# Kernel tuning notes

Measured on AMD Instinct MI355X. Metric: run time of the kernel, lower is better.

Reference implementation:

```python
import jax, jax.numpy as jnp
import numpy as np

K = 8
NUM_BLOCKS = 12

def knn_idx(xyz, k):
    # xyz: (B,3,N). kNN in Euclidean space (self included), like gutil.group.
    sq = jnp.sum(xyz * xyz, axis=1)                      # (B,N)
    inner = jnp.einsum('bdn,bdm->bnm', xyz, xyz)         # (B,N,N)
    dist = sq[:, :, None] - 2.0 * inner + sq[:, None, :]
    _, idx = jax.lax.top_k(-dist, k)                     # (B,N,k)
    return idx

def gather_neighbors(points, idx):
    # points: (B,d,N), idx: (B,N,k) -> grouped (B,d,k,N)  [gutil.group_point]
    g = jax.vmap(lambda p, i: p[:, i])(points, idx)      # (B,d,N,k)
    return jnp.transpose(g, (0, 1, 3, 2))

def setup_inputs() -> dict:
    key = jax.random.key(0)
    ks = jax.random.split(key, 6)
    B, N, D = 4, 4096, 128
    return {
        'xyz': jax.random.normal(ks[0], (B, 3, N), dtype=jnp.float32),
        'points': jax.random.normal(ks[1], (B, D, N), dtype=jnp.float32),
        'conv_w1': jax.random.normal(ks[2], (NUM_BLOCKS, D, D), dtype=jnp.float32) * 0.05,
        'conv_w2': jax.random.normal(ks[3], (NUM_BLOCKS, D, D), dtype=jnp.float32) * 0.05,
        'w_center': jax.random.normal(ks[4], (6, D), dtype=jnp.float32) * 0.05,
        'w_neighbor': jax.random.normal(ks[5], (6, D), dtype=jnp.float32) * 0.05,
    }

def reference(xyz, points, conv_w1, conv_w2, w_center, w_neighbor):
    # kNN indices depend only on xyz -> computed once (idx==0 branch in torch).
    idx = knn_idx(xyz, K)
    inv = 1.0 / (K + 1)
    for i in range(NUM_BLOCKS):
        shortcut = points
        p = jax.nn.relu(points)                              # (B,d,N)
        grouped = gather_neighbors(p, idx)                   # (B,d,K,N)
        center = jnp.einsum('oi,bin->bon', conv_w1[i], p)    # 1x1 conv on center
        gnn_sum = jnp.einsum('oi,bikn->bon', conv_w2[i], grouped)  # conv + sum over K
        # mean over concat([center(1), grouped(K)]) along neighbor dim + residual
        points = (center + gnn_sum) * inv + shortcut
        if i == NUM_BLOCKS - 1:
            pxyz = jnp.einsum('oi,bin->bon', w_center, p)            # (B,6,N)
            gxyz_sum = jnp.einsum('oi,bikn->bon', w_neighbor, grouped)
            new_xyz = (pxyz + gxyz_sum) * inv                        # (B,6,N)
            B, _, N = xyz.shape
            new_xyz = new_xyz.reshape(B, 3, 2, N) + xyz[:, :, None, :]
            new_xyz = new_xyz.reshape(B, 3, 2 * N)
            return (new_xyz, points)
```

## Files before the change

kernel.cpp:

```cpp
#include <hip/hip_runtime.h>
#include <math.h>

#define BB 4
#define NN 4096
#define DD 128
#define KK 8
#define NBLK 12

typedef __attribute__((ext_vector_type(8))) short short8;
typedef __attribute__((ext_vector_type(4))) float f32x4;

__device__ inline ushort bf16_rn(float x) {
    uint u = __float_as_uint(x);
    u = (u + 0x7FFFu + ((u >> 16) & 1u)) >> 16;
    return (ushort)u;
}
__device__ inline float bf16_f(ushort h) { return __uint_as_float(((uint)h) << 16); }

__global__ __launch_bounds__(512) void knn_kernel(const float* __restrict__ xyz,
                                                  int* __restrict__ idx) {
    __shared__ float xs[NN], ys[NN], zs[NN];
    const int b = blockIdx.y;
    const float* xb = xyz + (size_t)b * 3 * NN;
    for (int i = threadIdx.x; i < NN; i += 512) {
        xs[i] = xb[i];
        ys[i] = xb[NN + i];
        zs[i] = xb[2 * NN + i];
    }
    __syncthreads();

    const int wave = threadIdx.x >> 6;
    const int lane = threadIdx.x & 63;
    const int n = blockIdx.x * 8 + wave;
    const float qx = xs[n], qy = ys[n], qz = zs[n];
    const float qsq = __fadd_rn(__fadd_rn(__fmul_rn(qx, qx), __fmul_rn(qy, qy)),
                                __fmul_rn(qz, qz));

    float d[KK];
    int id[KK];
#pragma unroll
    for (int j = 0; j < KK; ++j) { d[j] = INFINITY; id[j] = -1; }

    for (int j = 0; j < NN / 256; ++j) {
        const int m0 = j * 256 + lane * 4;
        const float4 vx = *(const float4*)&xs[m0];
        const float4 vy = *(const float4*)&ys[m0];
        const float4 vz = *(const float4*)&zs[m0];
#pragma unroll
        for (int e = 0; e < 4; ++e) {
            const float cx = (&vx.x)[e], cy = (&vy.x)[e], cz = (&vz.x)[e];
            const float cq = __fadd_rn(__fadd_rn(__fmul_rn(cx, cx),
                                                 __fmul_rn(cy, cy)),
                                       __fmul_rn(cz, cz));
            float inner = __fadd_rn(__fadd_rn(__fmul_rn(qx, cx),
                                              __fmul_rn(qy, cy)),
                                    __fmul_rn(qz, cz));
            float dist = __fadd_rn(__fsub_rn(qsq, __fmul_rn(2.0f, inner)), cq);
            if (dist < d[KK - 1]) {
                d[KK - 1] = dist; id[KK - 1] = m0 + e;
#pragma unroll
                for (int t = KK - 1; t > 0; --t) {
                    if (d[t] < d[t - 1]) {
                        float td = d[t]; d[t] = d[t - 1]; d[t - 1] = td;
                        int ti = id[t]; id[t] = id[t - 1]; id[t - 1] = ti;
                    }
                }
            }
        }
    }

    int out[KK];
#pragma unroll
    for (int it = 0; it < KK; ++it) {
        float hd = d[0];
        int hi = id[0];
#pragma unroll
        for (int s = 32; s; s >>= 1) {
            float od = __shfl_xor(hd, s, 64);
            int oi = __shfl_xor(hi, s, 64);
            if (od < hd || (od == hd && oi < hi)) { hd = od; hi = oi; }
        }
        out[it] = hi;
        if (hd == d[0] && hi == id[0]) {
#pragma unroll
            for (int t = 0; t < KK - 1; ++t) { d[t] = d[t + 1]; id[t] = id[t + 1]; }
            d[KK - 1] = INFINITY; id[KK - 1] = -1;
        }
    }

    if (lane == 0) {
        int* op = idx + ((size_t)b * NN + n) * KK;
        *(int4*)op       = make_int4(out[0], out[1], out[2], out[3]);
        *(int4*)(op + 4) = make_int4(out[4], out[5], out[6], out[7]);
    }
}

__global__ __launch_bounds__(256) void prep_w(const float* __restrict__ w1,
                                              const float* __restrict__ w2,
                                              ushort* __restrict__ whi,
                                              ushort* __restrict__ wlo) {
    const int e = blockIdx.x * 256 + threadIdx.x;
    const int l = e >> 15;
    const int rem = e & 32767;
    const int r = rem >> 8;
    const int k = rem & 255;
    float w = (k < 128) ? w1[((size_t)l * 128 + r) * 128 + k]
                        : w2[((size_t)l * 128 + r) * 128 + (k - 128)];
    ushort h = bf16_rn(w);
    whi[e] = h;
    wlo[e] = bf16_rn(w - bf16_f(h));
}

__global__ __launch_bounds__(256) void transpose_pts(const float* __restrict__ pts,
                                                     float* __restrict__ ptsT) {
    __shared__ float t[32][33];
    const int b = blockIdx.z;
    const int c0 = blockIdx.y * 32;
    const int n0 = blockIdx.x * 32;
    const int tx = threadIdx.x & 31;
    const int ty = threadIdx.x >> 5;
#pragma unroll
    for (int q = 0; q < 4; ++q)
        t[ty + 8 * q][tx] = pts[((size_t)b * DD + c0 + ty + 8 * q) * NN + n0 + tx];
    __syncthreads();
#pragma unroll
    for (int q = 0; q < 4; ++q)
        ptsT[((size_t)b * NN + n0 + ty + 8 * q) * DD + c0 + tx] = t[tx][ty + 8 * q];
}

__global__ __launch_bounds__(512, 4) void fused_block(const float* __restrict__ ptsT_in,
                                                      const int* __restrict__ idx,
                                                      const ushort* __restrict__ whi,
                                                      const ushort* __restrict__ wlo,
                                                      float* __restrict__ ptsT_out,
                                                      float* __restrict__ out_std,
                                                      const float* __restrict__ wc,
                                                      const float* __restrict__ wn,
                                                      const float* __restrict__ xyz,
                                                      float* __restrict__ out_xyz,
                                                      const int last) {
    __shared__ __align__(16) char xt[32768];
    __shared__ float sc[32][132];
    char* xt_hi = xt;
    char* xt_lo = xt + 16384;

    const int bid = blockIdx.x;
    const int xcd = bid & 7;
    const int b = xcd >> 1;
    const int colbase = (((xcd & 1) << 6) + (bid >> 3)) * 32;

    const int w = threadIdx.x >> 6;
    const int lane = threadIdx.x & 63;
    const int half = lane >> 5;
    const int l32 = lane & 31;
    const int choff = 4 * l32;
    const int row0 = w * 4;

    const float* baseT = ptsT_in + (size_t)b * NN * DD;

    const int iv = idx[((size_t)b * NN + colbase + row0) * KK + (lane & 31)];

    const int ln15 = lane & 15;
    const int kl = lane >> 4;

#pragma unroll
    for (int i = 0; i < 2; ++i) {
        const int n_loc = row0 + 2 * i + half;
        const int n = colbase + n_loc;

        int nb[KK];
#pragma unroll
        for (int j = 0; j < KK; ++j) nb[j] = __shfl(iv, (2 * i + half) * 8 + j, 64);

        const float4 c4 = *(const float4*)(baseT + (size_t)n * DD + choff);
        float4 u[KK];
#pragma unroll
        for (int j = 0; j < KK; ++j)
            u[j] = *(const float4*)(baseT + (size_t)nb[j] * DD + choff);

        float g0 = 0.f, g1 = 0.f, g2 = 0.f, g3 = 0.f;
#pragma unroll
        for (int j = 0; j < KK; ++j) {
            g0 += fmaxf(u[j].x, 0.f);
            g1 += fmaxf(u[j].y, 0.f);
            g2 += fmaxf(u[j].z, 0.f);
            g3 += fmaxf(u[j].w, 0.f);
        }
        const float p0 = fmaxf(c4.x, 0.f);
        const float p1 = fmaxf(c4.y, 0.f);
        const float p2 = fmaxf(c4.z, 0.f);
        const float p3 = fmaxf(c4.w, 0.f);

        *(float4*)&sc[n_loc][choff] = c4;

        ushort ph0 = bf16_rn(p0), ph1 = bf16_rn(p1), ph2 = bf16_rn(p2), ph3 = bf16_rn(p3);
        ushort pl0 = bf16_rn(p0 - bf16_f(ph0)), pl1 = bf16_rn(p1 - bf16_f(ph1));
        ushort pl2 = bf16_rn(p2 - bf16_f(ph2)), pl3 = bf16_rn(p3 - bf16_f(ph3));
        ushort gh0 = bf16_rn(g0), gh1 = bf16_rn(g1), gh2 = bf16_rn(g2), gh3 = bf16_rn(g3);
        ushort gl0 = bf16_rn(g0 - bf16_f(gh0)), gl1 = bf16_rn(g1 - bf16_f(gh1));
        ushort gl2 = bf16_rn(g2 - bf16_f(gh2)), gl3 = bf16_rn(g3 - bf16_f(gh3));

        const int gP = l32 >> 1;
        const int sub = (l32 & 1) << 3;
        const int byP = n_loc * 512 + ((gP ^ (n_loc & 7)) << 4) + sub;
        const int byG = n_loc * 512 + (((16 + gP) ^ (n_loc & 7)) << 4) + sub;

        *(unsigned long long*)(xt_hi + byP) =
            (unsigned long long)ph0 | ((unsigned long long)ph1 << 16) |
            ((unsigned long long)ph2 << 32) | ((unsigned long long)ph3 << 48);
        *(unsigned long long*)(xt_lo + byP) =
            (unsigned long long)pl0 | ((unsigned long long)pl1 << 16) |
            ((unsigned long long)pl2 << 32) | ((unsigned long long)pl3 << 48);
        *(unsigned long long*)(xt_hi + byG) =
            (unsigned long long)gh0 | ((unsigned long long)gh1 << 16) |
            ((unsigned long long)gh2 << 32) | ((unsigned long long)gh3 << 48);
        *(unsigned long long*)(xt_lo + byG) =
            (unsigned long long)gl0 | ((unsigned long long)gl1 << 16) |
            ((unsigned long long)gl2 << 32) | ((unsigned long long)gl3 << 48);

        if (last) {
            float s0, s1, s2, s3, s4, s5;
            {
                const int c0 = choff, c1 = choff + 1, c2 = choff + 2, c3 = choff + 3;
                s0 = p0 * wc[0 * 128 + c0] + p1 * wc[0 * 128 + c1] + p2 * wc[0 * 128 + c2] + p3 * wc[0 * 128 + c3]
                   + g0 * wn[0 * 128 + c0] + g1 * wn[0 * 128 + c1] + g2 * wn[0 * 128 + c2] + g3 * wn[0 * 128 + c3];
                s1 = p0 * wc[1 * 128 + c0] + p1 * wc[1 * 128 + c1] + p2 * wc[1 * 128 + c2] + p3 * wc[1 * 128 + c3]
                   + g0 * wn[1 * 128 + c0] + g1 * wn[1 * 128 + c1] + g2 * wn[1 * 128 + c2] + g3 * wn[1 * 128 + c3];
                s2 = p0 * wc[2 * 128 + c0] + p1 * wc[2 * 128 + c1] + p2 * wc[2 * 128 + c2] + p3 * wc[2 * 128 + c3]
                   + g0 * wn[2 * 128 + c0] + g1 * wn[2 * 128 + c1] + g2 * wn[2 * 128 + c2] + g3 * wn[2 * 128 + c3];
                s3 = p0 * wc[3 * 128 + c0] + p1 * wc[3 * 128 + c1] + p2 * wc[3 * 128 + c2] + p3 * wc[3 * 128 + c3]
                   + g0 * wn[3 * 128 + c0] + g1 * wn[3 * 128 + c1] + g2 * wn[3 * 128 + c2] + g3 * wn[3 * 128 + c3];
                s4 = p0 * wc[4 * 128 + c0] + p1 * wc[4 * 128 + c1] + p2 * wc[4 * 128 + c2] + p3 * wc[4 * 128 + c3]
                   + g0 * wn[4 * 128 + c0] + g1 * wn[4 * 128 + c1] + g2 * wn[4 * 128 + c2] + g3 * wn[4 * 128 + c3];
                s5 = p0 * wc[5 * 128 + c0] + p1 * wc[5 * 128 + c1] + p2 * wc[5 * 128 + c2] + p3 * wc[5 * 128 + c3]
                   + g0 * wn[5 * 128 + c0] + g1 * wn[5 * 128 + c1] + g2 * wn[5 * 128 + c2] + g3 * wn[5 * 128 + c3];
            }
#pragma unroll
            for (int st = 16; st; st >>= 1) {
                s0 += __shfl_xor(s0, st, 64);
                s1 += __shfl_xor(s1, st, 64);
                s2 += __shfl_xor(s2, st, 64);
                s3 += __shfl_xor(s3, st, 64);
                s4 += __shfl_xor(s4, st, 64);
                s5 += __shfl_xor(s5, st, 64);
            }
            if (l32 < 6) {
                float v = s0;
                v = (l32 == 1) ? s1 : v;
                v = (l32 == 2) ? s2 : v;
                v = (l32 == 3) ? s3 : v;
                v = (l32 == 4) ? s4 : v;
                v = (l32 == 5) ? s5 : v;
                const int dd = l32 >> 1, h = l32 & 1;
                const float xv = xyz[((size_t)b * 3 + dd) * NN + n];
                out_xyz[(((size_t)b * 3 + dd) * 2 + h) * NN + n] =
                    v * (1.0f / 9.0f) + xv;
            }
        }
    }
    __syncthreads();

    const int wrow = w * 16 + ln15;
    f32x4 acc[2] = {};
#pragma unroll
    for (int ks = 0; ks < 8; ++ks) {
        const short8 a_hi = *(const short8*)(whi + (size_t)wrow * 256 + ks * 32 + kl * 8);
        const short8 a_lo = *(const short8*)(wlo + (size_t)wrow * 256 + ks * 32 + kl * 8);
        short8 bfh[2], bfl[2];
#pragma unroll
        for (int nt = 0; nt < 2; ++nt) {
            const int n_loc = nt * 16 + ln15;
            const int by = n_loc * 512 + (((ks * 4 + kl) ^ (n_loc & 7)) << 4);
            bfh[nt] = *(const short8*)(xt_hi + by);
            bfl[nt] = *(const short8*)(xt_lo + by);
        }
#pragma unroll
        for (int nt = 0; nt < 2; ++nt) {
            acc[nt] = __builtin_amdgcn_mfma_f32_16x16x32_bf16(a_hi, bfh[nt], acc[nt], 0, 0, 0);
            acc[nt] = __builtin_amdgcn_mfma_f32_16x16x32_bf16(a_hi, bfl[nt], acc[nt], 0, 0, 0);
            acc[nt] = __builtin_amdgcn_mfma_f32_16x16x32_bf16(a_lo, bfh[nt], acc[nt], 0, 0, 0);
        }
    }

    const float inv = 1.0f / 9.0f;
    const int orow = w * 16 + kl * 4;
#pragma unroll
    for (int nt = 0; nt < 2; ++nt) {
        const int nl = nt * 16 + ln15;
        const int n = colbase + nl;
        const float4 scv = *(const float4*)&sc[nl][orow];
        float v0 = acc[nt][0] * inv + scv.x;
        float v1 = acc[nt][1] * inv + scv.y;
        float v2 = acc[nt][2] * inv + scv.z;
        float v3 = acc[nt][3] * inv + scv.w;
        if (!last) {
            *(float4*)(ptsT_out + ((size_t)b * NN + n) * DD + orow) =
                make_float4(v0, v1, v2, v3);
        } else {
            out_std[((size_t)b * DD + orow + 0) * NN + n] = v0;
            out_std[((size_t)b * DD + orow + 1) * NN + n] = v1;
            out_std[((size_t)b * DD + orow + 2) * NN + n] = v2;
            out_std[((size_t)b * DD + orow + 3) * NN + n] = v3;
        }
    }
}

extern "C" void kernel_launch(void* const* d_in, const int* in_sizes, int n_in,
                              void* d_out, int out_size, void* d_ws, size_t ws_size,
                              hipStream_t stream) {
    const float* xyz    = (const float*)d_in[0];
    const float* points = (const float*)d_in[1];
    const float* w1     = (const float*)d_in[2];
    const float* w2     = (const float*)d_in[3];
    const float* wc     = (const float*)d_in[4];
    const float* wn     = (const float*)d_in[5];
    float* out = (float*)d_out;

    const size_t feat = (size_t)BB * DD * NN;
    char* ws = (char*)d_ws;
    int*    idx  = (int*)ws;
    ushort* whi  = (ushort*)(ws + 524288);
    ushort* wlo  = (ushort*)(ws + 524288 + 786432);
    float*  pT0  = (float*)(ws + 524288 + 2 * 786432);
    float*  pT1  = pT0 + feat;

    knn_kernel<<<dim3(NN / 8, BB), 512, 0, stream>>>(xyz, idx);
    prep_w<<<dim3(12 * 128 * 256 / 256), 256, 0, stream>>>(w1, w2, whi, wlo);
    transpose_pts<<<dim3(NN / 32, DD / 32, BB), 256, 0, stream>>>(points, pT0);

    float* out_pts = out + (size_t)BB * 3 * 2 * NN;
    float* bufs[2] = {pT0, pT1};
    for (int i = 0; i < NBLK; ++i) {
        const int last = (i == NBLK - 1);
        fused_block<<<dim3(512), 512, 0, stream>>>(
            bufs[i & 1], idx, whi + (size_t)i * 32768, wlo + (size_t)i * 32768,
            bufs[(i + 1) & 1], out_pts, wc, wn, xyz, out, last);
    }
}
```

Before: 276.5 us.

## Fuse twelve block launches into one persistent kernel with per-batch grid barriers

Replaces the twelve separate fused_block launches with a single persistent kernel that loops over the blocks internally. Between iterations, the workgroups for each batch synchronise through an atomic counter barrier in global memory, which replaces the kernel-launch boundaries. The goal is to remove launch overhead and the gaps between launches. It depends on all 512 workgroups being resident at the same time (a deadlock risk otherwise), and each barrier adds spin-wait latency plus a memset of the counters.

```diff
diff --git a/kernel.cpp b/kernel.cpp
--- a/kernel.cpp
+++ b/kernel.cpp
@@ -128,17 +128,17 @@
         ptsT[((size_t)b * NN + n0 + ty + 8 * q) * DD + c0 + tx] = t[tx][ty + 8 * q];
 }
 
-__global__ __launch_bounds__(512, 4) void fused_block(const float* __restrict__ ptsT_in,
+__global__ __launch_bounds__(512, 4) void fused_chain(float* __restrict__ pT0,
+                                                      float* __restrict__ pT1,
                                                       const int* __restrict__ idx,
                                                       const ushort* __restrict__ whi,
                                                       const ushort* __restrict__ wlo,
-                                                      float* __restrict__ ptsT_out,
                                                       float* __restrict__ out_std,
                                                       const float* __restrict__ wc,
                                                       const float* __restrict__ wn,
                                                       const float* __restrict__ xyz,
                                                       float* __restrict__ out_xyz,
-                                                      const int last) {
+                                                      unsigned int* ctr) {
     __shared__ __align__(16) char xt[32768];
     __shared__ float sc[32][132];
     char* xt_hi = xt;
@@ -156,151 +156,169 @@
     const int choff = 4 * l32;
     const int row0 = w * 4;
 
-    const float* baseT = ptsT_in + (size_t)b * NN * DD;
-
     const int iv = idx[((size_t)b * NN + colbase + row0) * KK + (lane & 31)];
 
     const int ln15 = lane & 15;
     const int kl = lane >> 4;
 
-#pragma unroll
-    for (int i = 0; i < 2; ++i) {
-        const int n_loc = row0 + 2 * i + half;
-        const int n = colbase + n_loc;
-
-        int nb[KK];
-#pragma unroll
-        for (int j = 0; j < KK; ++j) nb[j] = __shfl(iv, (2 * i + half) * 8 + j, 64);
-
-        const float4 c4 = *(const float4*)(baseT + (size_t)n * DD + choff);
-        float4 u[KK];
-#pragma unroll
-        for (int j = 0; j < KK; ++j)
-            u[j] = *(const float4*)(baseT + (size_t)nb[j] * DD + choff);
-
-        float g0 = 0.f, g1 = 0.f, g2 = 0.f, g3 = 0.f;
-#pragma unroll
-        for (int j = 0; j < KK; ++j) {
-            g0 += fmaxf(u[j].x, 0.f);
-            g1 += fmaxf(u[j].y, 0.f);
-            g2 += fmaxf(u[j].z, 0.f);
-            g3 += fmaxf(u[j].w, 0.f);
-        }
-        const float p0 = fmaxf(c4.x, 0.f);
-        const float p1 = fmaxf(c4.y, 0.f);
-        const float p2 = fmaxf(c4.z, 0.f);
-        const float p3 = fmaxf(c4.w, 0.f);
-
-        *(float4*)&sc[n_loc][choff] = c4;
-
-        ushort ph0 = bf16_rn(p0), ph1 = bf16_rn(p1), ph2 = bf16_rn(p2), ph3 = bf16_rn(p3);
-        ushort pl0 = bf16_rn(p0 - bf16_f(ph0)), pl1 = bf16_rn(p1 - bf16_f(ph1));
-        ushort pl2 = bf16_rn(p2 - bf16_f(ph2)), pl3 = bf16_rn(p3 - bf16_f(ph3));
-        ushort gh0 = bf16_rn(g0), gh1 = bf16_rn(g1), gh2 = bf16_rn(g2), gh3 = bf16_rn(g3);
-        ushort gl0 = bf16_rn(g0 - bf16_f(gh0)), gl1 = bf16_rn(g1 - bf16_f(gh1));
-        ushort gl2 = bf16_rn(g2 - bf16_f(gh2)), gl3 = bf16_rn(g3 - bf16_f(gh3));
-
-        const int gP = l32 >> 1;
-        const int sub = (l32 & 1) << 3;
-        const int byP = n_loc * 512 + ((gP ^ (n_loc & 7)) << 4) + sub;
-        const int byG = n_loc * 512 + (((16 + gP) ^ (n_loc & 7)) << 4) + sub;
-
-        *(unsigned long long*)(xt_hi + byP) =
-            (unsigned long long)ph0 | ((unsigned long long)ph1 << 16) |
-            ((unsigned long long)ph2 << 32) | ((unsigned long long)ph3 << 48);
-        *(unsigned long long*)(xt_lo + byP) =
-            (unsigned long long)pl0 | ((unsigned long long)pl1 << 16) |
-            ((unsigned long long)pl2 << 32) | ((unsigned long long)pl3 << 48);
-        *(unsigned long long*)(xt_hi + byG) =
-            (unsigned long long)gh0 | ((unsigned long long)gh1 << 16) |
-            ((unsigned long long)gh2 << 32) | ((unsigned long long)gh3 << 48);
-        *(unsigned long long*)(xt_lo + byG) =
-            (unsigned long long)gl0 | ((unsigned long long)gl1 << 16) |
-            ((unsigned long long)gl2 << 32) | ((unsigned long long)gl3 << 48);
-
-        if (last) {
-            float s0, s1, s2, s3, s4, s5;
-            {
-                const int c0 = choff, c1 = choff + 1, c2 = choff + 2, c3 = choff + 3;
-                s0 = p0 * wc[0 * 128 + c0] + p1 * wc[0 * 128 + c1] + p2 * wc[0 * 128 + c2] + p3 * wc[0 * 128 + c3]
-                   + g0 * wn[0 * 128 + c0] + g1 * wn[0 * 128 + c1] + g2 * wn[0 * 128 + c2] + g3 * wn[0 * 128 + c3];
-                s1 = p0 * wc[1 * 128 + c0] + p1 * wc[1 * 128 + c1] + p2 * wc[1 * 128 + c2] + p3 * wc[1 * 128 + c3]
-                   + g0 * wn[1 * 128 + c0] + g1 * wn[1 * 128 + c1] + g2 * wn[1 * 128 + c2] + g3 * wn[1 * 128 + c3];
-                s2 = p0 * wc[2 * 128 + c0] + p1 * wc[2 * 128 + c1] + p2 * wc[2 * 128 + c2] + p3 * wc[2 * 128 + c3]
-                   + g0 * wn[2 * 128 + c0] + g1 * wn[2 * 128 + c1] + g2 * wn[2 * 128 + c2] + g3 * wn[2 * 128 + c3];
-                s3 = p0 * wc[3 * 128 + c0] + p1 * wc[3 * 128 + c1] + p2 * wc[3 * 128 + c2] + p3 * wc[3 * 128 + c3]
-                   + g0 * wn[3 * 128 + c0] + g1 * wn[3 * 128 + c1] + g2 * wn[3 * 128 + c2] + g3 * wn[3 * 128 + c3];
-                s4 = p0 * wc[4 * 128 + c0] + p1 * wc[4 * 128 + c1] + p2 * wc[4 * 128 + c2] + p3 * wc[4 * 128 + c3]
-                   + g0 * wn[4 * 128 + c0] + g1 * wn[4 * 128 + c1] + g2 * wn[4 * 128 + c2] + g3 * wn[4 * 128 + c3];
-                s5 = p0 * wc[5 * 128 + c0] + p1 * wc[5 * 128 + c1] + p2 * wc[5 * 128 + c2] + p3 * wc[5 * 128 + c3]
-                   + g0 * wn[5 * 128 + c0] + g1 * wn[5 * 128 + c1] + g2 * wn[5 * 128 + c2] + g3 * wn[5 * 128 + c3];
-            }
-#pragma unroll
-            for (int st = 16; st; st >>= 1) {
-                s0 += __shfl_xor(s0, st, 64);
-                s1 += __shfl_xor(s1, st, 64);
-                s2 += __shfl_xor(s2, st, 64);
-                s3 += __shfl_xor(s3, st, 64);
-                s4 += __shfl_xor(s4, st, 64);
-                s5 += __shfl_xor(s5, st, 64);
-            }
-            if (l32 < 6) {
-                float v = s0;
-                v = (l32 == 1) ? s1 : v;
-                v = (l32 == 2) ? s2 : v;
-                v = (l32 == 3) ? s3 : v;
-                v = (l32 == 4) ? s4 : v;
-                v = (l32 == 5) ? s5 : v;
-                const int dd = l32 >> 1, h = l32 & 1;
-                const float xv = xyz[((size_t)b * 3 + dd) * NN + n];
-                out_xyz[(((size_t)b * 3 + dd) * 2 + h) * NN + n] =
-                    v * (1.0f / 9.0f) + xv;
-            }
-        }
-    }
-    __syncthreads();
-
-    const int wrow = w * 16 + ln15;
-    f32x4 acc[2] = {};
-#pragma unroll
-    for (int ks = 0; ks < 8; ++ks) {
-        const short8 a_hi = *(const short8*)(whi + (size_t)wrow * 256 + ks * 32 + kl * 8);
-        const short8 a_lo = *(const short8*)(wlo + (size_t)wrow * 256 + ks * 32 + kl * 8);
-        short8 bfh[2], bfl[2];
+    for (int it = 0; it < NBLK; ++it) {
+        const float* baseT = (it & 1 ? pT1 : pT0) + (size_t)b * NN * DD;
+        float* outT = (it & 1 ? pT0 : pT1);
+        const ushort* whi_i = whi + (size_t)it * 32768;
+        const ushort* wlo_i = wlo + (size_t)it * 32768;
+        const int last = (it == NBLK - 1);
+
+#pragma unroll
+        for (int i = 0; i < 2; ++i) {
+            const int n_loc = row0 + 2 * i + half;
+            const int n = colbase + n_loc;
+
+            int nb[KK];
+#pragma unroll
+            for (int j = 0; j < KK; ++j) nb[j] = __shfl(iv, (2 * i + half) * 8 + j, 64);
+
+            const float4 c4 = *(const float4*)(baseT + (size_t)n * DD + choff);
+            float4 u[KK];
+#pragma unroll
+            for (int j = 0; j < KK; ++j)
+                u[j] = *(const float4*)(baseT + (size_t)nb[j] * DD + choff);
+
+            float g0 = 0.f, g1 = 0.f, g2 = 0.f, g3 = 0.f;
+#pragma unroll
+            for (int j = 0; j < KK; ++j) {
+                g0 += fmaxf(u[j].x, 0.f);
+                g1 += fmaxf(u[j].y, 0.f);
+                g2 += fmaxf(u[j].z, 0.f);
+                g3 += fmaxf(u[j].w, 0.f);
+            }
+            const float p0 = fmaxf(c4.x, 0.f);
+            const float p1 = fmaxf(c4.y, 0.f);
+            const float p2 = fmaxf(c4.z, 0.f);
+            const float p3 = fmaxf(c4.w, 0.f);
+
+            *(float4*)&sc[n_loc][choff] = c4;
+
+            ushort ph0 = bf16_rn(p0), ph1 = bf16_rn(p1), ph2 = bf16_rn(p2), ph3 = bf16_rn(p3);
+            ushort pl0 = bf16_rn(p0 - bf16_f(ph0)), pl1 = bf16_rn(p1 - bf16_f(ph1));
+            ushort pl2 = bf16_rn(p2 - bf16_f(ph2)), pl3 = bf16_rn(p3 - bf16_f(ph3));
+            ushort gh0 = bf16_rn(g0), gh1 = bf16_rn(g1), gh2 = bf16_rn(g2), gh3 = bf16_rn(g3);
+            ushort gl0 = bf16_rn(g0 - bf16_f(gh0)), gl1 = bf16_rn(g1 - bf16_f(gh1));
+            ushort gl2 = bf16_rn(g2 - bf16_f(gh2)), gl3 = bf16_rn(g3 - bf16_f(gh3));
+
+            const int gP = l32 >> 1;
+            const int sub = (l32 & 1) << 3;
+            const int byP = n_loc * 512 + ((gP ^ (n_loc & 7)) << 4) + sub;
+            const int byG = n_loc * 512 + (((16 + gP) ^ (n_loc & 7)) << 4) + sub;
+
+            *(unsigned long long*)(xt_hi + byP) =
+                (unsigned long long)ph0 | ((unsigned long long)ph1 << 16) |
+                ((unsigned long long)ph2 << 32) | ((unsigned long long)ph3 << 48);
+            *(unsigned long long*)(xt_lo + byP) =
+                (unsigned long long)pl0 | ((unsigned long long)pl1 << 16) |
+                ((unsigned long long)pl2 << 32) | ((unsigned long long)pl3 << 48);
+            *(unsigned long long*)(xt_hi + byG) =
+                (unsigned long long)gh0 | ((unsigned long long)gh1 << 16) |
+                ((unsigned long long)gh2 << 32) | ((unsigned long long)gh3 << 48);
+            *(unsigned long long*)(xt_lo + byG) =
+                (unsigned long long)gl0 | ((unsigned long long)gl1 << 16) |
+                ((unsigned long long)gl2 << 32) | ((unsigned long long)gl3 << 48);
+
+            if (last) {
+                float s0, s1, s2, s3, s4, s5;
+                {
+                    const int c0 = choff, c1 = choff + 1, c2 = choff + 2, c3 = choff + 3;
+                    s0 = p0 * wc[0 * 128 + c0] + p1 * wc[0 * 128 + c1] + p2 * wc[0 * 128 + c2] + p3 * wc[0 * 128 + c3]
+                       + g0 * wn[0 * 128 + c0] + g1 * wn[0 * 128 + c1] + g2 * wn[0 * 128 + c2] + g3 * wn[0 * 128 + c3];
+                    s1 = p0 * wc[1 * 128 + c0] + p1 * wc[1 * 128 + c1] + p2 * wc[1 * 128 + c2] + p3 * wc[1 * 128 + c3]
+                       + g0 * wn[1 * 128 + c0] + g1 * wn[1 * 128 + c1] + g2 * wn[1 * 128 + c2] + g3 * wn[1 * 128 + c3];
+                    s2 = p0 * wc[2 * 128 + c0] + p1 * wc[2 * 128 + c1] + p2 * wc[2 * 128 + c2] + p3 * wc[2 * 128 + c3]
+                       + g0 * wn[2 * 128 + c0] + g1 * wn[2 * 128 + c1] + g2 * wn[2 * 128 + c2] + g3 * wn[2 * 128 + c3];
+                    s3 = p0 * wc[3 * 128 + c0] + p1 * wc[3 * 128 + c1] + p2 * wc[3 * 128 + c2] + p3 * wc[3 * 128 + c3]
+                       + g0 * wn[3 * 128 + c0] + g1 * wn[3 * 128 + c1] + g2 * wn[3 * 128 + c2] + g3 * wn[3 * 128 + c3];
+                    s4 = p0 * wc[4 * 128 + c0] + p1 * wc[4 * 128 + c1] + p2 * wc[4 * 128 + c2] + p3 * wc[4 * 128 + c3]
+                       + g0 * wn[4 * 128 + c0] + g1 * wn[4 * 128 + c1] + g2 * wn[4 * 128 + c2] + g3 * wn[4 * 128 + c3];
+                    s5 = p0 * wc[5 * 128 + c0] + p1 * wc[5 * 128 + c1] + p2 * wc[5 * 128 + c2] + p3 * wc[5 * 128 + c3]
+                       + g0 * wn[5 * 128 + c0] + g1 * wn[5 * 128 + c1] + g2 * wn[5 * 128 + c2] + g3 * wn[5 * 128 + c3];
+                }
+#pragma unroll
+                for (int st = 16; st; st >>= 1) {
+                    s0 += __shfl_xor(s0, st, 64);
+                    s1 += __shfl_xor(s1, st, 64);
+                    s2 += __shfl_xor(s2, st, 64);
+                    s3 += __shfl_xor(s3, st, 64);
+                    s4 += __shfl_xor(s4, st, 64);
+                    s5 += __shfl_xor(s5, st, 64);
+                }
+                if (l32 < 6) {
+                    float v = s0;
+                    v = (l32 == 1) ? s1 : v;
+                    v = (l32 == 2) ? s2 : v;
+                    v = (l32 == 3) ? s3 : v;
+                    v = (l32 == 4) ? s4 : v;
+                    v = (l32 == 5) ? s5 : v;
+                    const int dd = l32 >> 1, h = l32 & 1;
+                    const float xv = xyz[((size_t)b * 3 + dd) * NN + n];
+                    out_xyz[(((size_t)b * 3 + dd) * 2 + h) * NN + n] =
+                        v * (1.0f / 9.0f) + xv;
+                }
+            }
+        }
+        __syncthreads();
+
+        const int wrow = w * 16 + ln15;
+        f32x4 acc[2] = {};
+#pragma unroll
+        for (int ks = 0; ks < 8; ++ks) {
+            const short8 a_hi = *(const short8*)(whi_i + (size_t)wrow * 256 + ks * 32 + kl * 8);
+            const short8 a_lo = *(const short8*)(wlo_i + (size_t)wrow * 256 + ks * 32 + kl * 8);
+            short8 bfh[2], bfl[2];
+#pragma unroll
+            for (int nt = 0; nt < 2; ++nt) {
+                const int n_loc = nt * 16 + ln15;
+                const int by = n_loc * 512 + (((ks * 4 + kl) ^ (n_loc & 7)) << 4);
+                bfh[nt] = *(const short8*)(xt_hi + by);
+                bfl[nt] = *(const short8*)(xt_lo + by);
+            }
+#pragma unroll
+            for (int nt = 0; nt < 2; ++nt) {
+                acc[nt] = __builtin_amdgcn_mfma_f32_16x16x32_bf16(a_hi, bfh[nt], acc[nt], 0, 0, 0);
+                acc[nt] = __builtin_amdgcn_mfma_f32_16x16x32_bf16(a_hi, bfl[nt], acc[nt], 0, 0, 0);
+                acc[nt] = __builtin_amdgcn_mfma_f32_16x16x32_bf16(a_lo, bfh[nt], acc[nt], 0, 0, 0);
+            }
+        }
+
+        const float inv = 1.0f / 9.0f;
+        const int orow = w * 16 + kl * 4;
 #pragma unroll
         for (int nt = 0; nt < 2; ++nt) {
-            const int n_loc = nt * 16 + ln15;
-            const int by = n_loc * 512 + (((ks * 4 + kl) ^ (n_loc & 7)) << 4);
-            bfh[nt] = *(const short8*)(xt_hi + by);
-            bfl[nt] = *(const short8*)(xt_lo + by);
-        }
-#pragma unroll
-        for (int nt = 0; nt < 2; ++nt) {
-            acc[nt] = __builtin_amdgcn_mfma_f32_16x16x32_bf16(a_hi, bfh[nt], acc[nt], 0, 0, 0);
-            acc[nt] = __builtin_amdgcn_mfma_f32_16x16x32_bf16(a_hi, bfl[nt], acc[nt], 0, 0, 0);
-            acc[nt] = __builtin_amdgcn_mfma_f32_16x16x32_bf16(a_lo, bfh[nt], acc[nt], 0, 0, 0);
-        }
-    }
-
-    const float inv = 1.0f / 9.0f;
-    const int orow = w * 16 + kl * 4;
-#pragma unroll
-    for (int nt = 0; nt < 2; ++nt) {
-        const int nl = nt * 16 + ln15;
-        const int n = colbase + nl;
-        const float4 scv = *(const float4*)&sc[nl][orow];
-        float v0 = acc[nt][0] * inv + scv.x;
-        float v1 = acc[nt][1] * inv + scv.y;
-        float v2 = acc[nt][2] * inv + scv.z;
-        float v3 = acc[nt][3] * inv + scv.w;
-        if (!last) {
-            *(float4*)(ptsT_out + ((size_t)b * NN + n) * DD + orow) =
-                make_float4(v0, v1, v2, v3);
-        } else {
-            out_std[((size_t)b * DD + orow + 0) * NN + n] = v0;
-            out_std[((size_t)b * DD + orow + 1) * NN + n] = v1;
-            out_std[((size_t)b * DD + orow + 2) * NN + n] = v2;
-            out_std[((size_t)b * DD + orow + 3) * NN + n] = v3;
+            const int nl = nt * 16 + ln15;
+            const int n = colbase + nl;
+            const float4 scv = *(const float4*)&sc[nl][orow];
+            float v0 = acc[nt][0] * inv + scv.x;
+            float v1 = acc[nt][1] * inv + scv.y;
+            float v2 = acc[nt][2] * inv + scv.z;
+            float v3 = acc[nt][3] * inv + scv.w;
+            if (!last) {
+                *(float4*)(outT + ((size_t)b * NN + n) * DD + orow) =
+                    make_float4(v0, v1, v2, v3);
+            } else {
+                out_std[((size_t)b * DD + orow + 0) * NN + n] = v0;
+                out_std[((size_t)b * DD + orow + 1) * NN + n] = v1;
+                out_std[((size_t)b * DD + orow + 2) * NN + n] = v2;
+                out_std[((size_t)b * DD + orow + 3) * NN + n] = v3;
+            }
+        }
+
+        if (it < NBLK - 1) {
+            __syncthreads();
+            if (threadIdx.x == 0) {
+                __threadfence();
+                atomicAdd(&ctr[it * 4 + b], 1u);
+                while (atomicAdd(&ctr[it * 4 + b], 0u) < 128u)
+                    __builtin_amdgcn_s_sleep(32);
+                __threadfence();
+            }
+            __syncthreads();
         }
     }
 }
@@ -320,20 +338,18 @@
     char* ws = (char*)d_ws;
     int*    idx  = (int*)ws;
     ushort* whi  = (ushort*)(ws + 524288);
-    ushort* wlo  = (ushort*)(ws + 524288 + 786432);
-    float*  pT0  = (float*)(ws + 524288 + 2 * 786432);
+    ushort* wlo  = (ushort*)(ws + 1310720);
+    float*  pT0  = (float*)(ws + 2097152);
     float*  pT1  = pT0 + feat;
+    unsigned int* ctr = (unsigned int*)(ws + 2097152 + 2 * feat * sizeof(float));
+
+    hipMemsetAsync(ctr, 0, 4 * (NBLK) * sizeof(unsigned int), stream);
 
     knn_kernel<<<dim3(NN / 8, BB), 512, 0, stream>>>(xyz, idx);
     prep_w<<<dim3(12 * 128 * 256 / 256), 256, 0, stream>>>(w1, w2, whi, wlo);
     transpose_pts<<<dim3(NN / 32, DD / 32, BB), 256, 0, stream>>>(points, pT0);
 
     float* out_pts = out + (size_t)BB * 3 * 2 * NN;
-    float* bufs[2] = {pT0, pT1};
-    for (int i = 0; i < NBLK; ++i) {
-        const int last = (i == NBLK - 1);
-        fused_block<<<dim3(512), 512, 0, stream>>>(
-            bufs[i & 1], idx, whi + (size_t)i * 32768, wlo + (size_t)i * 32768,
-            bufs[(i + 1) & 1], out_pts, wc, wn, xyz, out, last);
-    }
-}
+    fused_chain<<<dim3(512), 512, 0, stream>>>(
+        pT0, pT1, idx, whi, wlo, out_pts, wc, wn, xyz, out, ctr);
+}
```

Measured after the change: 810.3 us. 193% more time.
